# Optimization experiments

Hardware: AMD Instinct MI355X
Metric: run time of the kernel (lower is better)

Reference implementation:

```python
import jax, jax.numpy as jnp
import numpy as np

N_NODES = 8192
N_EDGES = 262144
D_IN = 512
D_OUT = 512


def setup_inputs() -> dict:
    key = jax.random.key(0)
    k1, k2, k3 = jax.random.split(key, 3)
    x = jax.random.normal(k1, (N_NODES, D_IN), dtype=jnp.float32)
    edge_index = jax.random.randint(k2, (2, N_EDGES), 0, N_NODES, dtype=jnp.int64)
    weight = jax.random.normal(k3, (D_IN, D_OUT), dtype=jnp.float32)
    bias = jnp.zeros((D_OUT,), dtype=jnp.float32)
    return {"x": x, "edge_index": edge_index, "weight": weight, "bias": bias}


def reference(x, edge_index, weight, bias):
    # GCN layer with selfloop=True branch of the original module.
    n = x.shape[0]
    # Dense symmetric adjacency via scatter-set, matching adj[ei0,ei1]=1; adj[ei1,ei0]=1
    adj = jnp.zeros((n, n), dtype=x.dtype)
    adj = adj.at[edge_index[0], edge_index[1]].set(1.0)
    adj = adj.at[edge_index[1], edge_index[0]].set(1.0)
    # Add self loops, symmetric degree normalization D^{-1/2} A D^{-1/2}
    adj = adj + jnp.eye(n, dtype=x.dtype)
    deg = jnp.sum(adj, axis=1)
    dinv = 1.0 / jnp.sqrt(deg)
    adj = adj * dinv[:, None] * dinv[None, :]  # == D @ adj @ D (diagonal scaling)
    return adj @ (x @ weight) + bias
```

## Files before the change

kernel.cpp:

```cpp
#include <hip/hip_runtime.h>
#include <hip/hip_bf16.h>


#define ELL_STRIDE 128

typedef __attribute__((ext_vector_type(8))) short bf16x8;
typedef __attribute__((ext_vector_type(4))) float f32x4;
typedef __attribute__((ext_vector_type(2))) float f32x2;

__device__ __forceinline__ unsigned short f2bf(float f) {
  unsigned u = __float_as_uint(f);
  u = (u + 0x7fff + ((u >> 16) & 1)) >> 16;
  return (unsigned short)u;
}
__device__ __forceinline__ float bflo(unsigned u) {
  return __uint_as_float(u << 16);
}
__device__ __forceinline__ float bfhi(unsigned u) {
  return __uint_as_float(u & 0xffff0000u);
}

__global__ __launch_bounds__(256) void fused_front_kernel(
    const int* __restrict__ ei, unsigned* __restrict__ mask, int n_edges,
    int words,
    const float* __restrict__ x, unsigned short* __restrict__ xb, int n4,
    const float* __restrict__ W, unsigned short* __restrict__ Wt, int K, int N,
    unsigned short* __restrict__ Hs, float* __restrict__ dinv, int n_nodes,
    int edge_blocks, int cast_blocks, int tr_blocks) {
  const int bid = blockIdx.x;
  if (bid < edge_blocks) {
    const int e = bid * 256 + threadIdx.x;
    if (e < n_edges) {
      const int u = ei[e];
      const int v = ei[e + n_edges];
      atomicOr(&mask[(size_t)u * words + (v >> 5)], 1u << (v & 31));
      atomicOr(&mask[(size_t)v * words + (u >> 5)], 1u << (u & 31));
    }
    return;
  }
  if (bid < edge_blocks + cast_blocks) {
    const int t = (bid - edge_blocks) * 256 + threadIdx.x;
    if (t < n4) {
      float4 v = ((const float4*)x)[t];
      ushort4 o;
      o.x = f2bf(v.x); o.y = f2bf(v.y); o.z = f2bf(v.z); o.w = f2bf(v.w);
      ((ushort4*)xb)[t] = o;
    }
    return;
  }
  if (bid < edge_blocks + cast_blocks + tr_blocks) {
    __shared__ float tile[32][33];
    const int b = bid - edge_blocks - cast_blocks;
    const int bx = b & ((N >> 5) - 1);
    const int by = b >> (31 - __builtin_clz(N >> 5));
    const int tx = threadIdx.x & 31;
    const int ty = threadIdx.x >> 5;
#pragma unroll
    for (int r = 0; r < 4; ++r)
      tile[ty + 8 * r][tx] = W[(size_t)(by * 32 + ty + 8 * r) * N + bx * 32 + tx];
    __syncthreads();
#pragma unroll
    for (int r = 0; r < 4; ++r)
      Wt[(size_t)(bx * 32 + ty + 8 * r) * K + by * 32 + tx] =
          f2bf(tile[tx][ty + 8 * r]);
    return;
  }
  {
    const int t = threadIdx.x;
    if (t < (N >> 1)) ((unsigned*)(Hs + (size_t)n_nodes * N))[t] = 0;
    if (t == 0) dinv[n_nodes] = 0.f;
  }
}

__global__ __launch_bounds__(256) void fused_mid_kernel(
    const unsigned short* __restrict__ xb,
    const unsigned short* __restrict__ Wt,
    unsigned short* __restrict__ Hs,
    const unsigned* __restrict__ mask, unsigned short* __restrict__ ell,
    int* __restrict__ deg, float* __restrict__ dinv,
    int M, int N, int K, int words, int gemm_blocks, int nbx_sh) {
  __shared__ unsigned short As[512 * 8];
  __shared__ unsigned short Bs[1024 * 8];

  const int tid = threadIdx.x;
  const int bid = blockIdx.x;

  if (bid < gemm_blocks) {
    const int wave = tid >> 6;
    const int lane = tid & 63;
    const int q = lane >> 4;
    const int c = lane & 15;
    const int bx = bid & ((1 << nbx_sh) - 1);
    const int by = bid >> nbx_sh;
    const int m0 = by * 64;
    const int n0 = bx * 128;
    const int wr = wave >> 1, wc = wave & 1;

    f32x4 acc[2][4] = {};

    for (int k0 = 0; k0 < K; k0 += 64) {
#pragma unroll
      for (int t = 0; t < 2; ++t) {
        const int sbase = t * 256 + wave * 64;
        const int s = sbase + lane;
        const unsigned short* g =
            xb + (size_t)(m0 + (s & 63)) * K + k0 + (s >> 6) * 8;
        __builtin_amdgcn_global_load_lds(
            (const __attribute__((address_space(1))) void*)g,
            (__attribute__((address_space(3))) void*)(As + sbase * 8), 16, 0, 0);
      }
#pragma unroll
      for (int t = 0; t < 4; ++t) {
        const int sbase = t * 256 + wave * 64;
        const int s = sbase + lane;
        const int bn = s >> 3;
        const int bk = (s & 7) ^ (bn & 7);
        const unsigned short* g =
            Wt + (size_t)(n0 + bn) * K + k0 + bk * 8;
        __builtin_amdgcn_global_load_lds(
            (const __attribute__((address_space(1))) void*)g,
            (__attribute__((address_space(3))) void*)(Bs + sbase * 8), 16, 0, 0);
      }
      __syncthreads();

#pragma unroll
      for (int kk = 0; kk < 2; ++kk) {
        bf16x8 a[2], b[4];
#pragma unroll
        for (int tm = 0; tm < 2; ++tm) {
          const int row = wr * 32 + tm * 16 + c;
          a[tm] = *(const bf16x8*)(As + (((kk * 4 + q) * 64) + row) * 8);
        }
#pragma unroll
        for (int tn = 0; tn < 4; ++tn) {
          const int n = wc * 64 + tn * 16 + c;
          b[tn] = *(const bf16x8*)(Bs + (n * 8 + ((kk * 4 + q) ^ (n & 7))) * 8);
        }
#pragma unroll
        for (int tm = 0; tm < 2; ++tm)
#pragma unroll
          for (int tn = 0; tn < 4; ++tn)
            acc[tm][tn] = __builtin_amdgcn_mfma_f32_16x16x32_bf16(
                a[tm], b[tn], acc[tm][tn], 0, 0, 0);
      }
      __syncthreads();
    }

#pragma unroll
    for (int tm = 0; tm < 2; ++tm) {
#pragma unroll
      for (int r = 0; r < 4; ++r) {
        const int grow = m0 + wr * 32 + tm * 16 + q * 4 + r;
#pragma unroll
        for (int tn = 0; tn < 4; ++tn) {
          const int gcol = n0 + wc * 64 + tn * 16 + c;
          Hs[(size_t)grow * N + gcol] = f2bf(acc[tm][tn][r]);
        }
      }
    }
    return;
  }

  {
    const int wave = tid >> 6, lane = tid & 63;
    const int node = (bid - gemm_blocks) * 4 + wave;
    const unsigned* __restrict__ row = mask + (size_t)node * words;
    unsigned short* __restrict__ out = ell + (size_t)node * ELL_STRIDE;

    int running = 0;
    for (int r = 0; r < words; r += 64) {
      const int w = r + lane;
      unsigned bits = row[w];
      const int cnt = __popc(bits);
      int x = cnt;
#pragma unroll
      for (int d = 1; d < 64; d <<= 1) {
        int y = __shfl_up(x, d, 64);
        if (lane >= d) x += y;
      }
      int pos = running + x - cnt;
      while (bits) {
        const int b = __builtin_ctz(bits);
        bits &= bits - 1;
        if (pos < ELL_STRIDE) out[pos] = (unsigned short)((w << 5) + b);
        ++pos;
      }
      running += __shfl(x, 63, 64);
    }
    for (int p = running + lane; p < ELL_STRIDE; p += 64)
      out[p] = (unsigned short)(p == running ? node : M);
    if (lane == 0) {
      const int dd = running + 1;
      deg[node] = dd < ELL_STRIDE ? dd : ELL_STRIDE;
      dinv[node] = rsqrtf((float)running + 1.0f);
    }
  }
}

__global__ __launch_bounds__(1024) void spmm_kernel(
    const unsigned short* __restrict__ ell, const int* __restrict__ deg,
    const float* __restrict__ dinv, const unsigned short* __restrict__ Hs,
    const float* __restrict__ bias, float* __restrict__ out, int n, int D) {
  __shared__ float sdinv[8193];
  __shared__ uint2 ji[16][ELL_STRIDE];
  const int tid = threadIdx.x;
  const int wave = tid >> 6, lane = tid & 63;
  const int bid = blockIdx.x;
  const int qt = bid & 3;
  const int i = (bid >> 2) * 16 + wave;
  const unsigned rowbytes = (unsigned)(D * 2);

  for (int t = tid; t < n + 1; t += 1024) sdinv[t] = dinv[t];
  __syncthreads();

  {
    const unsigned j0 = ell[(size_t)i * ELL_STRIDE + lane];
    const unsigned j1 = ell[(size_t)i * ELL_STRIDE + 64 + lane];
    ji[wave][lane] = make_uint2(j0 * rowbytes, __float_as_uint(sdinv[j0]));
    ji[wave][64 + lane] = make_uint2(j1 * rowbytes, __float_as_uint(sdinv[j1]));
  }
  const int d = deg[i];
  const float di = sdinv[i];
  const int kmax = (d + 7) & ~7;

  const char* __restrict__ hb = (const char*)Hs + qt * 256 + lane * 4;
  float a0 = 0.f, a1 = 0.f;

#pragma unroll 8
  for (int k = 0; k < kmax; ++k) {
    const uint2 e = ji[wave][k];
    const float dj = __uint_as_float(e.y);
    const unsigned hv = *(const unsigned*)(hb + e.x);
    a0 += dj * bflo(hv);
    a1 += dj * bfhi(hv);
  }

  const int col = qt * (D >> 2) + lane * 2;
  const float2 b = *(const float2*)(bias + col);
  f32x2 o;
  o.x = di * a0 + b.x;
  o.y = di * a1 + b.y;
  __builtin_nontemporal_store(o, (f32x2*)(out + (size_t)i * D + col));
}

extern "C" void kernel_launch(void* const* d_in, const int* in_sizes, int n_in,
                              void* d_out, int out_size, void* d_ws, size_t ws_size,
                              hipStream_t stream) {
  const float* x    = (const float*)d_in[0];
  const int*   ei   = (const int*)d_in[1];
  const float* W    = (const float*)d_in[2];
  const float* bias = (const float*)d_in[3];
  float* out = (float*)d_out;

  const int d_out_dim = in_sizes[3];
  const int d_in_dim  = in_sizes[2] / d_out_dim;
  const int n_nodes   = in_sizes[0] / d_in_dim;
  const int n_edges   = in_sizes[1] / 2;
  const int words     = (n_nodes + 31) / 32;

  char* ws = (char*)d_ws;
  size_t off = 0;
  unsigned* mask = (unsigned*)(ws + off); off += (size_t)n_nodes * words * 4;
  int* deg       = (int*)(ws + off);      off += (size_t)n_nodes * 4;
  float* dinv    = (float*)(ws + off);    off += (size_t)(n_nodes + 1) * 4;
  unsigned short* ell = (unsigned short*)(ws + off); off += (size_t)n_nodes * ELL_STRIDE * 2;
  unsigned short* xb  = (unsigned short*)(ws + off); off += (size_t)n_nodes * d_in_dim * 2;
  unsigned short* Wt  = (unsigned short*)(ws + off); off += (size_t)d_in_dim * d_out_dim * 2;
  unsigned short* Hs  = (unsigned short*)(ws + off);
  off += (size_t)(n_nodes + 1) * d_out_dim * 2;

  hipMemsetAsync(mask, 0, (size_t)n_nodes * words * 4, stream);

  const int edge_blocks = (n_edges + 255) / 256;
  const int n4 = n_nodes * d_in_dim / 4;
  const int cast_blocks = (n4 + 255) / 256;
  const int tr_blocks = (d_in_dim / 32) * (d_out_dim / 32);
  fused_front_kernel<<<edge_blocks + cast_blocks + tr_blocks + 1, 256, 0, stream>>>(
      ei, mask, n_edges, words, x, xb, n4, W, Wt, d_in_dim, d_out_dim,
      Hs, dinv, n_nodes, edge_blocks, cast_blocks, tr_blocks);

  const int nbx = d_out_dim / 128;
  const int nbx_sh = 31 - __builtin_clz(nbx);
  const int gemm_blocks = nbx * (n_nodes / 64);
  const int ell_blocks = n_nodes / 4;
  fused_mid_kernel<<<gemm_blocks + ell_blocks, 256, 0, stream>>>(
      xb, Wt, Hs, mask, ell, deg, dinv,
      n_nodes, d_out_dim, d_in_dim, words, gemm_blocks, nbx_sh);

  const int spmm_blocks = 4 * (n_nodes / 16);
  spmm_kernel<<<spmm_blocks, 1024, 0, stream>>>(ell, deg, dinv, Hs, bias, out,
                                                n_nodes, d_out_dim);
}
```

Before: 150.7 us.

## Split adjacency build into own kernel, skip unused ELL half, unroll SpMM more

Moves the edge-scatter atomics out of the fused front kernel into a separate adj_kernel launch, which now issues each atomicOr twice (redundant, idempotent). In the SpMM kernel the second half of the ELL row is loaded only when degree exceeds 64, and the gather loop unroll rises from 8 to 16. The extra launch adds overhead and the duplicated atomics add memory traffic, while the conditional load saves a little bandwidth for low-degree rows.

```diff
diff --git a/kernel.cpp b/kernel.cpp
--- a/kernel.cpp
+++ b/kernel.cpp
@@ -20,26 +20,31 @@
   return __uint_as_float(u & 0xffff0000u);
 }
 
-__global__ __launch_bounds__(256) void fused_front_kernel(
+__global__ __launch_bounds__(256) void adj_kernel(
     const int* __restrict__ ei, unsigned* __restrict__ mask, int n_edges,
-    int words,
+    int words) {
+  const int e = blockIdx.x * 256 + threadIdx.x;
+  if (e >= n_edges) return;
+  const int u = ei[e];
+  const int v = ei[e + n_edges];
+  unsigned* au = &mask[(size_t)u * words + (v >> 5)];
+  unsigned* av = &mask[(size_t)v * words + (u >> 5)];
+  const unsigned bu = 1u << (v & 31);
+  const unsigned bv = 1u << (u & 31);
+  atomicOr(au, bu);
+  atomicOr(av, bv);
+  atomicOr(av, bv);
+  atomicOr(au, bu);
+}
+
+__global__ __launch_bounds__(256) void prep_kernel(
     const float* __restrict__ x, unsigned short* __restrict__ xb, int n4,
     const float* __restrict__ W, unsigned short* __restrict__ Wt, int K, int N,
     unsigned short* __restrict__ Hs, float* __restrict__ dinv, int n_nodes,
-    int edge_blocks, int cast_blocks, int tr_blocks) {
+    int cast_blocks, int tr_blocks) {
   const int bid = blockIdx.x;
-  if (bid < edge_blocks) {
-    const int e = bid * 256 + threadIdx.x;
-    if (e < n_edges) {
-      const int u = ei[e];
-      const int v = ei[e + n_edges];
-      atomicOr(&mask[(size_t)u * words + (v >> 5)], 1u << (v & 31));
-      atomicOr(&mask[(size_t)v * words + (u >> 5)], 1u << (u & 31));
-    }
-    return;
-  }
-  if (bid < edge_blocks + cast_blocks) {
-    const int t = (bid - edge_blocks) * 256 + threadIdx.x;
+  if (bid < cast_blocks) {
+    const int t = bid * 256 + threadIdx.x;
     if (t < n4) {
       float4 v = ((const float4*)x)[t];
       ushort4 o;
@@ -48,9 +53,9 @@
     }
     return;
   }
-  if (bid < edge_blocks + cast_blocks + tr_blocks) {
+  if (bid < cast_blocks + tr_blocks) {
     __shared__ float tile[32][33];
-    const int b = bid - edge_blocks - cast_blocks;
+    const int b = bid - cast_blocks;
     const int bx = b & ((N >> 5) - 1);
     const int by = b >> (31 - __builtin_clz(N >> 5));
     const int tx = threadIdx.x & 31;
@@ -210,23 +215,25 @@
   const int i = (bid >> 2) * 16 + wave;
   const unsigned rowbytes = (unsigned)(D * 2);
 
+  const int d = deg[i];
   for (int t = tid; t < n + 1; t += 1024) sdinv[t] = dinv[t];
   __syncthreads();
 
   {
     const unsigned j0 = ell[(size_t)i * ELL_STRIDE + lane];
-    const unsigned j1 = ell[(size_t)i * ELL_STRIDE + 64 + lane];
     ji[wave][lane] = make_uint2(j0 * rowbytes, __float_as_uint(sdinv[j0]));
-    ji[wave][64 + lane] = make_uint2(j1 * rowbytes, __float_as_uint(sdinv[j1]));
-  }
-  const int d = deg[i];
+    if (d >= 65) {
+      const unsigned j1 = ell[(size_t)i * ELL_STRIDE + 64 + lane];
+      ji[wave][64 + lane] = make_uint2(j1 * rowbytes, __float_as_uint(sdinv[j1]));
+    }
+  }
   const float di = sdinv[i];
   const int kmax = (d + 7) & ~7;
 
   const char* __restrict__ hb = (const char*)Hs + qt * 256 + lane * 4;
   float a0 = 0.f, a1 = 0.f;
 
-#pragma unroll 8
+#pragma unroll 16
   for (int k = 0; k < kmax; ++k) {
     const uint2 e = ji[wave][k];
     const float dj = __uint_as_float(e.y);
@@ -272,12 +279,14 @@
   hipMemsetAsync(mask, 0, (size_t)n_nodes * words * 4, stream);
 
   const int edge_blocks = (n_edges + 255) / 256;
+  adj_kernel<<<edge_blocks, 256, 0, stream>>>(ei, mask, n_edges, words);
+
   const int n4 = n_nodes * d_in_dim / 4;
   const int cast_blocks = (n4 + 255) / 256;
   const int tr_blocks = (d_in_dim / 32) * (d_out_dim / 32);
-  fused_front_kernel<<<edge_blocks + cast_blocks + tr_blocks + 1, 256, 0, stream>>>(
-      ei, mask, n_edges, words, x, xb, n4, W, Wt, d_in_dim, d_out_dim,
-      Hs, dinv, n_nodes, edge_blocks, cast_blocks, tr_blocks);
+  prep_kernel<<<cast_blocks + tr_blocks + 1, 256, 0, stream>>>(
+      x, xb, n4, W, Wt, d_in_dim, d_out_dim, Hs, dinv, n_nodes,
+      cast_blocks, tr_blocks);
 
   const int nbx = d_out_dim / 128;
   const int nbx_sh = 31 - __builtin_clz(nbx);
```

Result: slower. 178.5 us (+18.5%).
